# Performance work log

Hardware: AMD Instinct MI355X
Metric: run time of the kernel (lower is better)

The kernel has to match this reference:

```python
import jax, jax.numpy as jnp
import numpy as np

VERY_NEG = -1e30
N_HEADS = 8


def _dag_attention(leaves, ancestors, mask, w1, b1, w2, b2):
    # leaves/ancestors: [C, A, H], mask: [C, A]
    m = mask[..., None]                                   # [C, A, 1]
    x = jnp.concatenate([leaves * m, ancestors * m], -1)  # [C, A, 2H]
    x = jax.nn.relu(x @ w1 + b1)                          # [C, A, H]
    s = x @ w2 + b2 + (1.0 - m) * VERY_NEG                # [C, A, 1]
    a = jax.nn.softmax(s, axis=1)
    return (a * ancestors * m).sum(axis=1)                # [C, H]


def _encoder_layer(x, mask4d, wq, wk, wv, wo, fw1, fb1, fw2, fb2):
    B, S, H = x.shape
    d = H // N_HEADS
    q = (x @ wq).reshape(B, S, N_HEADS, d)
    k = (x @ wk).reshape(B, S, N_HEADS, d)
    v = (x @ wv).reshape(B, S, N_HEADS, d)
    scores = jnp.einsum('bqhd,bkhd->bhqk', q, k) / jnp.sqrt(jnp.float32(d)) + mask4d
    attn = jax.nn.softmax(scores, axis=-1)
    ctx = jnp.einsum('bhqk,bkhd->bqhd', attn, v).reshape(B, S, H)
    x = x + ctx @ wo
    x = x + jax.nn.relu(x @ fw1 + fb1) @ fw2 + fb2
    return x


def _attention_pooling(x, mask3d, pw, pb):
    # x: [B, S, H], mask3d: [B, S, 1] additive mask
    s = x @ pw + pb + mask3d           # [B, S, 1]
    a = jax.nn.softmax(s, axis=1)
    return (a * x).sum(axis=1)          # [B, H]


def setup_inputs() -> dict:
    key = jax.random.key(0)
    ks = jax.random.split(key, 32)
    B, S, H, C, NODES, A = 128, 256, 256, 20000, 25000, 8

    def w(k, shape, scale=0.02):
        return (jax.random.normal(k, shape, jnp.float32) * scale)

    input_ids = jax.random.randint(ks[0], (B, S), 0, C)
    code_mask = (jax.random.uniform(ks[1], (B, S)) < 0.9).astype(jnp.float32)
    code_mask = code_mask.at[:, 0].set(1.0)
    dx_leaves_list = jax.random.randint(ks[2], (C, A), 0, NODES)
    dx_ancestors_list = jax.random.randint(ks[3], (C, A), 0, NODES)
    dx_masks_list = (jax.random.uniform(ks[4], (C, A)) < 0.8).astype(jnp.float32)
    dx_masks_list = dx_masks_list.at[:, 0].set(1.0)

    inp = dict(
        input_ids=input_ids, code_mask=code_mask,
        dx_leaves_list=dx_leaves_list, dx_ancestors_list=dx_ancestors_list,
        dx_masks_list=dx_masks_list,
        embed_init_w=w(ks[5], (NODES + 1, H)).at[NODES].set(0.0),  # padding row
        embed_inputs_w=w(ks[6], (C + 1, H)).at[C].set(0.0),
        attn_w1=w(ks[7], (2 * H, H)), attn_b1=jnp.zeros((H,), jnp.float32),
        attn_w2=w(ks[8], (H, 1)), attn_b2=jnp.zeros((1,), jnp.float32),
        pool_w=w(ks[9], (H, 1)), pool_b=jnp.zeros((1,), jnp.float32),
    )
    names = ['visit', 'dag']
    for i, nm in enumerate(names):
        base = 10 + 6 * i
        inp[nm + '_wq'] = w(ks[base], (H, H))
        inp[nm + '_wk'] = w(ks[base + 1], (H, H))
        inp[nm + '_wv'] = w(ks[base + 2], (H, H))
        inp[nm + '_wo'] = w(ks[base + 3], (H, H))
        inp[nm + '_fw1'] = w(ks[base + 4], (H, 4 * H))
        inp[nm + '_fb1'] = jnp.zeros((4 * H,), jnp.float32)
        inp[nm + '_fw2'] = w(ks[base + 5], (4 * H, H))
        inp[nm + '_fb2'] = jnp.zeros((H,), jnp.float32)
    return inp


def reference(input_ids, code_mask, dx_leaves_list, dx_ancestors_list, dx_masks_list,
              embed_init_w, embed_inputs_w, attn_w1, attn_b1, attn_w2, attn_b2,
              pool_w, pool_b,
              visit_wq, visit_wk, visit_wv, visit_wo, visit_fw1, visit_fb1, visit_fw2, visit_fb2,
              dag_wq, dag_wk, dag_wv, dag_wo, dag_fw1, dag_fb1, dag_fw2, dag_fb2):
    H = embed_init_w.shape[1]
    # Full-vocabulary DAG embedding recomputation (gather -> MLP -> masked softmax -> weighted sum)
    leaves_emb = embed_init_w[dx_leaves_list]          # [C, A, H]
    ancestors_emb = embed_init_w[dx_ancestors_list]    # [C, A, H]
    dag_emb = _dag_attention(leaves_emb, ancestors_emb, dx_masks_list,
                             attn_w1, attn_b1, attn_w2, attn_b2)   # [C, H]
    dict_matrix = jnp.concatenate([jnp.zeros((1, H), jnp.float32), dag_emb], axis=0)

    inputs = embed_inputs_w[input_ids]       # [B, S, H]
    inputs_dag = dict_matrix[input_ids]      # [B, S, H]

    ext_mask = (1.0 - code_mask)[:, None, None, :] * VERY_NEG  # [B,1,1,S]
    visit_outs = _encoder_layer(inputs, ext_mask, visit_wq, visit_wk, visit_wv, visit_wo,
                                visit_fw1, visit_fb1, visit_fw2, visit_fb2)
    dag_hidden = _encoder_layer(inputs_dag, ext_mask, dag_wq, dag_wk, dag_wv, dag_wo,
                                dag_fw1, dag_fb1, dag_fw2, dag_fb2)

    pool_mask = (1.0 - code_mask)[:, :, None] * VERY_NEG       # [B,S,1]
    dag_outs = _attention_pooling(dag_hidden, pool_mask, pool_w, pool_b)
    return (visit_outs, dag_outs)
```

## Files before the change

### kernel.cpp

```cpp
#include <hip/hip_runtime.h>
#include <hip/hip_bf16.h>
#include <math.h>

#define VERY_NEG (-1e30f)

constexpr int Bc = 128, Sc = 256, Hc = 256, Cc = 20000, Ac = 8, NHc = 8, DHc = 32, FFc = 1024;
constexpr int Mc = Bc * Sc;
constexpr int Rc = Cc * Ac;

typedef __attribute__((ext_vector_type(8))) short short8;
typedef __attribute__((ext_vector_type(4))) float floatx4;

static __device__ __forceinline__ unsigned short f2bf(float f) {
  union { float f; unsigned u; } v; v.f = f;
  unsigned r = v.u + 0x7FFF + ((v.u >> 16) & 1);
  return (unsigned short)(r >> 16);
}
static __device__ __forceinline__ unsigned pack2(float lo, float hi) {
  return (unsigned)f2bf(lo) | ((unsigned)f2bf(hi) << 16);
}
static __device__ __forceinline__ float bf2f(unsigned short u) {
  union { unsigned u; float f; } v; v.u = ((unsigned)u) << 16; return v.f;
}

static __device__ __forceinline__ void glds16(const unsigned short* g,
                                              unsigned short* l) {
  __builtin_amdgcn_global_load_lds(
      (const __attribute__((address_space(1))) void*)g,
      (__attribute__((address_space(3))) void*)l, 16, 0, 0);
}

__global__ __launch_bounds__(256) void prep_weights(
    const float* __restrict__ wq, const float* __restrict__ wk,
    const float* __restrict__ wv, const float* __restrict__ wo,
    const float* __restrict__ fw1, const float* __restrict__ fw2,
    unsigned short* __restrict__ qkvT, unsigned short* __restrict__ woT,
    unsigned short* __restrict__ fw1T, unsigned short* __restrict__ fw2T) {
  int gid = blockIdx.x * 256 + threadIdx.x;
  if (gid < 196608) {
    int which = gid >> 16, rem = gid & 65535;
    int n = rem >> 8, k = rem & 255;
    const float* w = which == 0 ? wq : (which == 1 ? wk : wv);
    qkvT[gid] = f2bf(w[k * 256 + n]);
  } else if (gid < 262144) {
    int rem = gid - 196608;
    int n = rem >> 8, k = rem & 255;
    woT[rem] = f2bf(wo[k * 256 + n]);
  } else if (gid < 524288) {
    int rem = gid - 262144;
    int n = rem >> 8, k = rem & 255;
    fw1T[rem] = f2bf(fw1[k * 1024 + n]);
  } else {
    int rem = gid - 524288;
    int n = rem >> 10, k = rem & 1023;
    fw2T[rem] = f2bf(fw2[k * 256 + n]);
  }
}

template <int K, bool BIAS, bool RELU, bool RESID, int OUT>
__global__ __launch_bounds__(256) void gemm_mfma(
    const unsigned short* __restrict__ A, const unsigned short* __restrict__ Bt,
    const float* __restrict__ bias, const float* __restrict__ resid,
    float* __restrict__ Cf, unsigned short* __restrict__ C2, int N) {
  __shared__ unsigned short As[128 * 64];
  __shared__ unsigned short Bs[128 * 64];
  const int tid = threadIdx.x;
  const int rowBase = blockIdx.y * 128;
  const int colBase = blockIdx.x * 128;
  const int wave = tid >> 6, lane = tid & 63;
  const int wm = wave >> 1, wn = wave & 1;
  const int quad = lane >> 4, l15 = lane & 15;
  const int s8 = (((lane & 7) ^ (lane >> 3)) << 3);
  const int rs0 = (wave << 5) + (lane >> 3);
  const int swz = l15 & 7;

  floatx4 acc[4][4];
#pragma unroll
  for (int mt = 0; mt < 4; ++mt)
#pragma unroll
    for (int nt = 0; nt < 4; ++nt) acc[mt][nt] = (floatx4){0.f, 0.f, 0.f, 0.f};

  for (int k0 = 0; k0 < K; k0 += 64) {
#pragma unroll
    for (int i = 0; i < 4; ++i) {
      int r = rs0 + (i << 3);
      int lb = wave * 2048 + i * 512;
      glds16(A + (size_t)(rowBase + r) * K + k0 + s8, &As[lb]);
      glds16(Bt + (size_t)(colBase + r) * K + k0 + s8, &Bs[lb]);
    }
    __syncthreads();
#pragma unroll
    for (int kk = 0; kk < 2; ++kk) {
      short8 af[4], bfr[4];
#pragma unroll
      for (int mt = 0; mt < 4; ++mt)
        af[mt] = *(const short8*)&As[(wm * 64 + mt * 16 + l15) * 64 +
                                     ((((kk << 2) | quad) ^ swz) << 3)];
#pragma unroll
      for (int nt = 0; nt < 4; ++nt)
        bfr[nt] = *(const short8*)&Bs[(wn * 64 + nt * 16 + l15) * 64 +
                                      ((((kk << 2) | quad) ^ swz) << 3)];
#pragma unroll
      for (int mt = 0; mt < 4; ++mt)
#pragma unroll
        for (int nt = 0; nt < 4; ++nt)
          acc[mt][nt] = __builtin_amdgcn_mfma_f32_16x16x32_bf16(
              af[mt], bfr[nt], acc[mt][nt], 0, 0, 0);
    }
    __syncthreads();
  }

#pragma unroll
  for (int mt = 0; mt < 4; ++mt) {
#pragma unroll
    for (int nt = 0; nt < 4; ++nt) {
      int col = colBase + wn * 64 + nt * 16 + l15;
      float bz = BIAS ? bias[col] : 0.f;
#pragma unroll
      for (int i = 0; i < 4; ++i) {
        int row = rowBase + wm * 64 + mt * 16 + quad * 4 + i;
        float v = acc[mt][nt][i];
        if (BIAS) v += bz;
        if (RELU) v = fmaxf(v, 0.f);
        if (RESID) v += resid[(size_t)row * N + col];
        if (OUT == 0) {
          Cf[(size_t)row * N + col] = v;
        } else if (OUT == 1) {
          C2[(size_t)row * N + col] = f2bf(v);
        } else if (OUT == 2) {
          Cf[(size_t)row * N + col] = v;
          C2[(size_t)row * N + col] = f2bf(v);
        } else {
          C2[(size_t)(col >> 8) * 16777216 + (size_t)row * 256 + (col & 255)] =
              f2bf(v);
        }
      }
    }
  }
}

__global__ __launch_bounds__(256) void cvt_emb16(
    const float* __restrict__ emb, unsigned short* __restrict__ e16) {
  int gid = blockIdx.x * 256 + threadIdx.x;
  int base = gid * 8;
  int row = base >> 8;
  uint4 o;
  if (row < 25001) {
    float4 a = *(const float4*)(emb + base);
    float4 b = *(const float4*)(emb + base + 4);
    o.x = pack2(a.x, a.y); o.y = pack2(a.z, a.w);
    o.z = pack2(b.x, b.y); o.w = pack2(b.z, b.w);
  } else {
    o = (uint4){0u, 0u, 0u, 0u};
  }
  *(uint4*)(e16 + base) = o;
}

__global__ __launch_bounds__(256) void prep_w1T_pq(
    const float* __restrict__ w1, unsigned short* __restrict__ Bt) {
  int gid = blockIdx.x * 256 + threadIdx.x;
  int n = gid >> 8, k = gid & 255;
  float v = (n < 256) ? w1[k * 256 + n] : w1[(256 + k) * 256 + (n - 256)];
  Bt[gid] = f2bf(v);
}

__global__ __launch_bounds__(256) void dag_score(
    const int* __restrict__ leaves, const int* __restrict__ anc,
    const unsigned short* __restrict__ PQ, const float* __restrict__ b1,
    const float* __restrict__ w2, float* __restrict__ s) {
  const int tid = threadIdx.x;
  const int l16 = tid & 15;
  const int r = blockIdx.x * 16 + (tid >> 4);

  float b1c[16], w2c[16];
#pragma unroll
  for (int j = 0; j < 4; ++j) {
    *(float4*)&b1c[j * 4] = *(const float4*)(b1 + l16 * 16 + j * 4);
    *(float4*)&w2c[j * 4] = *(const float4*)(w2 + l16 * 16 + j * 4);
  }

  const int nl = leaves[r], na = anc[r];
  const unsigned short* pp = PQ + (size_t)nl * 512 + l16 * 16;
  const unsigned short* qp = PQ + (size_t)na * 512 + 256 + l16 * 16;

  float acc = 0.f;
#pragma unroll
  for (int half = 0; half < 2; ++half) {
    uint4 pv = *(const uint4*)(pp + half * 8);
    uint4 qv = *(const uint4*)(qp + half * 8);
    const unsigned short* pu = (const unsigned short*)&pv;
    const unsigned short* qu = (const unsigned short*)&qv;
#pragma unroll
    for (int j = 0; j < 8; ++j) {
      float h = bf2f(pu[j]) + bf2f(qu[j]) + b1c[half * 8 + j];
      acc += fmaxf(h, 0.f) * w2c[half * 8 + j];
    }
  }
  acc += __shfl_xor(acc, 1, 64);
  acc += __shfl_xor(acc, 2, 64);
  acc += __shfl_xor(acc, 4, 64);
  acc += __shfl_xor(acc, 8, 64);
  if (l16 == 0) s[r] = acc;
}

__global__ __launch_bounds__(256) void dag_finalize(
    const float* __restrict__ s, const float* __restrict__ masks,
    const int* __restrict__ anc, const float* __restrict__ b2,
    const float* __restrict__ emb, float* __restrict__ dict) {
  const int c = blockIdx.x;
  const int t = threadIdx.x;
  __shared__ float sv[8], mv[8];
  __shared__ int nv[8];
  if (t < 8) {
    int idx = c * 8 + t;
    float m = masks[idx];
    sv[t] = s[idx] + b2[0] + (1.f - m) * VERY_NEG;
    mv[t] = m;
    nv[t] = anc[idx];
  }
  __syncthreads();
  float mx = -INFINITY;
#pragma unroll
  for (int a = 0; a < 8; ++a) mx = fmaxf(mx, sv[a]);
  float e[8], sum = 0.f;
#pragma unroll
  for (int a = 0; a < 8; ++a) { e[a] = __expf(sv[a] - mx); sum += e[a]; }
  float inv = 1.f / sum;
  float o = 0.f;
#pragma unroll
  for (int a = 0; a < 8; ++a)
    o += e[a] * inv * mv[a] * emb[(size_t)nv[a] * 256 + t];
  dict[(size_t)(c + 1) * 256 + t] = o;
  if (c == 0) dict[t] = 0.f;
}

__global__ __launch_bounds__(256) void gather_both(
    const int* __restrict__ ids, const float4* __restrict__ table,
    float4* __restrict__ outf, unsigned short* __restrict__ outb) {
  int gid = blockIdx.x * 256 + threadIdx.x;
  int row = gid >> 6;
  int c4 = gid & 63;
  float4 v = table[(size_t)ids[row] * 64 + c4];
  outf[gid] = v;
  uint2 o;
  o.x = pack2(v.x, v.y);
  o.y = pack2(v.z, v.w);
  *(uint2*)(outb + (size_t)gid * 4) = o;
}

__global__ __launch_bounds__(256) void attn_mfma(
    const unsigned short* __restrict__ q, const unsigned short* __restrict__ k,
    const unsigned short* __restrict__ v, const float* __restrict__ cm,
    unsigned short* __restrict__ ctx) {
  __shared__ unsigned short Vt[32][264];
  __shared__ unsigned short Ps[4][64][68];
  __shared__ float madd[256];
  const int b = blockIdx.x >> 3, h = blockIdx.x & 7;
  const int tid = threadIdx.x;
  const int wave = tid >> 6, lane = tid & 63;
  const int quad = lane >> 4, l15 = lane & 15;
  const size_t tokbase = (size_t)b * 256;
  const int hoff = h * 32;

  unsigned short* Vtmp = &Ps[0][0][0];

#pragma unroll
  for (int it = 0; it < 4; ++it) {
    int idx = tid + it * 256;
    int row = idx >> 2, c = idx & 3;
    size_t g = (tokbase + row) * 256 + hoff + c * 8;
    *(uint4*)(Vtmp + row * 40 + c * 8) = *(const uint4*)(v + g);
  }
  madd[tid] = (1.f - cm[b * 256 + tid]) * VERY_NEG;
  __syncthreads();
#pragma unroll
  for (int it = 0; it < 4; ++it) {
    int idx = tid + it * 256;
    int row = idx & 255, c = idx >> 8;
    uint4 w = *(const uint4*)(Vtmp + row * 40 + c * 8);
    const unsigned short* wsp = (const unsigned short*)&w;
#pragma unroll
    for (int j = 0; j < 8; ++j) Vt[c * 8 + j][row] = wsp[j];
  }
  __syncthreads();

  short8 qf[4];
#pragma unroll
  for (int mt = 0; mt < 4; ++mt) {
    size_t qrow = tokbase + wave * 64 + mt * 16 + l15;
    qf[mt] = *(const short8*)(q + qrow * 256 + hoff + quad * 8);
  }
  float madd_r[16];
#pragma unroll
  for (int nt = 0; nt < 16; ++nt) madd_r[nt] = madd[nt * 16 + l15];

  float l_r[4][4];
  floatx4 oa[4][2];
#pragma unroll
  for (int mt = 0; mt < 4; ++mt)
#pragma unroll
    for (int i = 0; i < 4; ++i) l_r[mt][i] = 0.f;
#pragma unroll
  for (int mt = 0; mt < 4; ++mt)
#pragma unroll
    for (int nd = 0; nd < 2; ++nd) oa[mt][nd] = (floatx4){0.f, 0.f, 0.f, 0.f};

  const float scale = 0.17677669529663687f;

  for (int t = 0; t < 4; ++t) {
    short8 kf[4];
#pragma unroll
    for (int nt = 0; nt < 4; ++nt)
      kf[nt] = *(const short8*)(k + (tokbase + t * 64 + nt * 16 + l15) * 256 +
                                hoff + quad * 8);
    floatx4 sa[4][4];
#pragma unroll
    for (int mt = 0; mt < 4; ++mt)
#pragma unroll
      for (int nt = 0; nt < 4; ++nt) sa[mt][nt] = (floatx4){0.f, 0.f, 0.f, 0.f};
#pragma unroll
    for (int mt = 0; mt < 4; ++mt)
#pragma unroll
      for (int nt = 0; nt < 4; ++nt)
        sa[mt][nt] = __builtin_amdgcn_mfma_f32_16x16x32_bf16(
            qf[mt], kf[nt], sa[mt][nt], 0, 0, 0);

#pragma unroll
    for (int mt = 0; mt < 4; ++mt) {
#pragma unroll
      for (int i = 0; i < 4; ++i) {
        float rs = 0.f;
#pragma unroll
        for (int nt = 0; nt < 4; ++nt) {
          float p = __expf(sa[mt][nt][i] * scale + madd_r[t * 4 + nt]);
          sa[mt][nt][i] = p;
          rs += p;
        }
        rs += __shfl_xor(rs, 1, 64);
        rs += __shfl_xor(rs, 2, 64);
        rs += __shfl_xor(rs, 4, 64);
        rs += __shfl_xor(rs, 8, 64);
        l_r[mt][i] += rs;
      }
    }
#pragma unroll
    for (int mt = 0; mt < 4; ++mt)
#pragma unroll
      for (int nt = 0; nt < 4; ++nt)
#pragma unroll
        for (int i = 0; i < 4; ++i)
          Ps[wave][mt * 16 + quad * 4 + i][nt * 16 + l15] =
              f2bf(sa[mt][nt][i]);
    __asm__ __volatile__("s_waitcnt lgkmcnt(0)" ::: "memory");
#pragma unroll
    for (int ks = 0; ks < 2; ++ks) {
      short8 vf[2];
#pragma unroll
      for (int nd = 0; nd < 2; ++nd)
        vf[nd] =
            *(const short8*)&Vt[nd * 16 + l15][t * 64 + ks * 32 + quad * 8];
#pragma unroll
      for (int mt = 0; mt < 4; ++mt) {
        short8 pf = *(const short8*)&Ps[wave][mt * 16 + l15][ks * 32 + quad * 8];
#pragma unroll
        for (int nd = 0; nd < 2; ++nd)
          oa[mt][nd] = __builtin_amdgcn_mfma_f32_16x16x32_bf16(
              pf, vf[nd], oa[mt][nd], 0, 0, 0);
      }
    }
    __asm__ __volatile__("s_waitcnt lgkmcnt(0)" ::: "memory");
  }

  unsigned short* OsW = &Ps[wave][0][0];
#pragma unroll
  for (int mt = 0; mt < 4; ++mt)
#pragma unroll
    for (int nd = 0; nd < 2; ++nd)
#pragma unroll
      for (int i = 0; i < 4; ++i)
        OsW[(mt * 16 + quad * 4 + i) * 40 + nd * 16 + l15] =
            f2bf(oa[mt][nd][i] / l_r[mt][i]);
  __asm__ __volatile__("s_waitcnt lgkmcnt(0)" ::: "memory");
#pragma unroll
  for (int it = 0; it < 4; ++it) {
    int idx = it * 64 + lane;
    int row = idx >> 2, c = idx & 3;
    uint4 w = *(const uint4*)(OsW + row * 40 + c * 8);
    *(uint4*)(ctx + (tokbase + wave * 64 + row) * 256 + hoff + c * 8) = w;
  }
}

__global__ __launch_bounds__(256) void pool_kernel(
    const float* __restrict__ x, const float* __restrict__ code_mask,
    const float* __restrict__ pw, const float* __restrict__ pb,
    float* __restrict__ out) {
  const int b = blockIdx.x;
  const int t = threadIdx.x;
  __shared__ float ss[256];
  __shared__ float red[256];
  __shared__ float als[256];
  const float* xb = x + (size_t)b * 256 * 256;

  float s = pb[0];
  for (int j = 0; j < 256; j += 4) {
    float4 xv = *(const float4*)(xb + (size_t)t * 256 + j);
    float4 wv = *(const float4*)(pw + j);
    s += xv.x * wv.x + xv.y * wv.y + xv.z * wv.z + xv.w * wv.w;
  }
  s += (1.f - code_mask[b * 256 + t]) * VERY_NEG;
  ss[t] = s; red[t] = s;
  __syncthreads();
  for (int off = 128; off > 0; off >>= 1) {
    if (t < off) red[t] = fmaxf(red[t], red[t + off]);
    __syncthreads();
  }
  float m = red[0];
  __syncthreads();
  float e = __expf(ss[t] - m);
  als[t] = e; red[t] = e;
  __syncthreads();
  for (int off = 128; off > 0; off >>= 1) {
    if (t < off) red[t] += red[t + off];
    __syncthreads();
  }
  float inv = 1.f / red[0];
  float o = 0.f;
  for (int si = 0; si < 256; ++si) o += als[si] * xb[(size_t)si * 256 + t];
  out[b * 256 + t] = o * inv;
}

extern "C" void kernel_launch(void* const* d_in, const int* in_sizes, int n_in,
                              void* d_out, int out_size, void* d_ws,
                              size_t ws_size, hipStream_t stream) {
  const int* input_ids = (const int*)d_in[0];
  const float* code_mask = (const float*)d_in[1];
  const int* dx_leaves = (const int*)d_in[2];
  const int* dx_anc = (const int*)d_in[3];
  const float* dx_masks = (const float*)d_in[4];
  const float* embed_init_w = (const float*)d_in[5];
  const float* embed_inputs_w = (const float*)d_in[6];
  const float* attn_w1 = (const float*)d_in[7];
  const float* attn_b1 = (const float*)d_in[8];
  const float* attn_w2 = (const float*)d_in[9];
  const float* attn_b2 = (const float*)d_in[10];
  const float* pool_w = (const float*)d_in[11];
  const float* pool_b = (const float*)d_in[12];

  float* out = (float*)d_out;
  float* ws = (float*)d_ws;

  float* dict = ws;
  float* xbuf = dict + 5120256;
  float* qb   = xbuf + 8388608;
  float* kb   = qb + 8388608;
  float* vb   = kb + 8388608;
  float* ctxb = vb + 8388608;
  float* wend = ctxb + 8388608;

  unsigned short* emb16  = (unsigned short*)xbuf;
  unsigned short* pq16   = (unsigned short*)(xbuf + 3211264);
  unsigned short* w1T_pq = (unsigned short*)kb;
  float* sbuf = vb;

  unsigned short* xb16  = (unsigned short*)ctxb;
  unsigned short* qkv16 = (unsigned short*)qb;
  unsigned short* xq16  = (unsigned short*)qb;
  unsigned short* hid16 = (unsigned short*)kb;
  unsigned short* qkvT = (unsigned short*)wend;
  unsigned short* woT  = qkvT + 196608;
  unsigned short* fw1T = woT + 65536;
  unsigned short* fw2T = fw1T + 262144;

  cvt_emb16<<<3136, 256, 0, stream>>>(embed_init_w, emb16);
  prep_w1T_pq<<<512, 256, 0, stream>>>(attn_w1, w1T_pq);
  gemm_mfma<256, false, false, false, 1><<<dim3(4, 196), 256, 0, stream>>>(
      emb16, w1T_pq, nullptr, nullptr, nullptr, pq16, 512);
  dag_score<<<Rc / 16, 256, 0, stream>>>(dx_leaves, dx_anc, pq16, attn_b1,
                                         attn_w2, sbuf);
  dag_finalize<<<Cc, 256, 0, stream>>>(sbuf, dx_masks, dx_anc, attn_b2,
                                       embed_init_w, dict);

  auto run_encoder = [&](const float* wq, const float* wk, const float* wv,
                         const float* wo, const float* fw1, const float* fb1,
                         const float* fw2, const float* fb2, float* final_out) {
    prep_weights<<<3072, 256, 0, stream>>>(wq, wk, wv, wo, fw1, fw2, qkvT,
                                           woT, fw1T, fw2T);
    gemm_mfma<256, false, false, false, 3><<<dim3(6, 256), 256, 0, stream>>>(
        xb16, qkvT, nullptr, nullptr, nullptr, qkv16, 256);
    attn_mfma<<<Bc * NHc, 256, 0, stream>>>(qkv16, qkv16 + 16777216,
                                            qkv16 + 33554432, code_mask, xb16);
    gemm_mfma<256, false, false, true, 2><<<dim3(2, 256), 256, 0, stream>>>(
        xb16, woT, nullptr, xbuf, xbuf, xq16, 256);
    gemm_mfma<256, true, true, false, 1><<<dim3(8, 256), 256, 0, stream>>>(
        xq16, fw1T, fb1, nullptr, nullptr, hid16, 1024);
    gemm_mfma<1024, true, false, true, 0><<<dim3(2, 256), 256, 0, stream>>>(
        hid16, fw2T, fb2, xbuf, final_out, nullptr, 256);
  };

  gather_both<<<8192, 256, 0, stream>>>(input_ids,
                                        (const float4*)embed_inputs_w,
                                        (float4*)xbuf, xb16);
  run_encoder((const float*)d_in[13], (const float*)d_in[14],
              (const float*)d_in[15], (const float*)d_in[16],
              (const float*)d_in[17], (const float*)d_in[18],
              (const float*)d_in[19], (const float*)d_in[20], out);

  gather_both<<<8192, 256, 0, stream>>>(input_ids, (const float4*)dict,
                                        (float4*)xbuf, xb16);
  run_encoder((const float*)d_in[21], (const float*)d_in[22],
              (const float*)d_in[23], (const float*)d_in[24],
              (const float*)d_in[25], (const float*)d_in[26],
              (const float*)d_in[27], (const float*)d_in[28], xbuf);

  pool_kernel<<<Bc, 256, 0, stream>>>(xbuf, code_mask, pool_w, pool_b,
                                      out + 8388608);
}
```

Measured before the change: 605.2 us.

## Swizzle attention LDS layouts and compute softmax denominators via MFMA

Measured after the change: 582.3 us. 1.04x faster.

```diff
diff --git a/kernel.cpp b/kernel.cpp
--- a/kernel.cpp
+++ b/kernel.cpp
@@ -248,12 +248,19 @@
   *(uint2*)(outb + (size_t)gid * 4) = o;
 }
 
-__global__ __launch_bounds__(256) void attn_mfma(
+static __device__ __forceinline__ int vt_addr(int d, int col) {
+  return d * 272 + ((((col) * 2) ^ (((d >> 3) & 3) << 4)) >> 1);
+}
+static __device__ __forceinline__ int ps_addr(int row, int col) {
+  return row * 40 + ((((col) * 2) ^ (((row >> 2) & 3) << 4)) >> 1);
+}
+
+__global__ __launch_bounds__(256, 4) void attn_mfma(
     const unsigned short* __restrict__ q, const unsigned short* __restrict__ k,
     const unsigned short* __restrict__ v, const float* __restrict__ cm,
     unsigned short* __restrict__ ctx) {
-  __shared__ unsigned short Vt[32][264];
-  __shared__ unsigned short Ps[4][64][68];
+  __shared__ unsigned short Vt[32 * 272];
+  __shared__ unsigned short Ps[4][64 * 40];
   __shared__ float madd[256];
   const int b = blockIdx.x >> 3, h = blockIdx.x & 7;
   const int tid = threadIdx.x;
@@ -262,26 +269,16 @@
   const size_t tokbase = (size_t)b * 256;
   const int hoff = h * 32;
 
-  unsigned short* Vtmp = &Ps[0][0][0];
-
 #pragma unroll
   for (int it = 0; it < 4; ++it) {
     int idx = tid + it * 256;
     int row = idx >> 2, c = idx & 3;
-    size_t g = (tokbase + row) * 256 + hoff + c * 8;
-    *(uint4*)(Vtmp + row * 40 + c * 8) = *(const uint4*)(v + g);
+    uint4 w = *(const uint4*)(v + (tokbase + row) * 256 + hoff + c * 8);
+    const unsigned short* wsp = (const unsigned short*)&w;
+#pragma unroll
+    for (int j = 0; j < 8; ++j) Vt[vt_addr(c * 8 + j, row)] = wsp[j];
   }
   madd[tid] = (1.f - cm[b * 256 + tid]) * VERY_NEG;
-  __syncthreads();
-#pragma unroll
-  for (int it = 0; it < 4; ++it) {
-    int idx = tid + it * 256;
-    int row = idx & 255, c = idx >> 8;
-    uint4 w = *(const uint4*)(Vtmp + row * 40 + c * 8);
-    const unsigned short* wsp = (const unsigned short*)&w;
-#pragma unroll
-    for (int j = 0; j < 8; ++j) Vt[c * 8 + j][row] = wsp[j];
-  }
   __syncthreads();
 
   short8 qf[4];
@@ -294,18 +291,21 @@
 #pragma unroll
   for (int nt = 0; nt < 16; ++nt) madd_r[nt] = madd[nt * 16 + l15];
 
-  float l_r[4][4];
-  floatx4 oa[4][2];
-#pragma unroll
-  for (int mt = 0; mt < 4; ++mt)
-#pragma unroll
-    for (int i = 0; i < 4; ++i) l_r[mt][i] = 0.f;
-#pragma unroll
-  for (int mt = 0; mt < 4; ++mt)
+  short8 vone;
+#pragma unroll
+  for (int j = 0; j < 8; ++j)
+    ((unsigned short*)&vone)[j] = (l15 == 0) ? 0x3F80 : 0;
+
+  floatx4 oa[4][2], oa_l[4];
+#pragma unroll
+  for (int mt = 0; mt < 4; ++mt) {
+    oa_l[mt] = (floatx4){0.f, 0.f, 0.f, 0.f};
 #pragma unroll
     for (int nd = 0; nd < 2; ++nd) oa[mt][nd] = (floatx4){0.f, 0.f, 0.f, 0.f};
+  }
 
   const float scale = 0.17677669529663687f;
+  unsigned short* Pw = &Ps[wave][0];
 
   for (int t = 0; t < 4; ++t) {
     short8 kf[4];
@@ -326,66 +326,59 @@
             qf[mt], kf[nt], sa[mt][nt], 0, 0, 0);
 
 #pragma unroll
-    for (int mt = 0; mt < 4; ++mt) {
-#pragma unroll
-      for (int i = 0; i < 4; ++i) {
-        float rs = 0.f;
-#pragma unroll
-        for (int nt = 0; nt < 4; ++nt) {
-          float p = __expf(sa[mt][nt][i] * scale + madd_r[t * 4 + nt]);
-          sa[mt][nt][i] = p;
-          rs += p;
+    for (int ks = 0; ks < 2; ++ks) {
+#pragma unroll
+      for (int mt = 0; mt < 4; ++mt)
+#pragma unroll
+        for (int n2 = 0; n2 < 2; ++n2) {
+          int nt = ks * 2 + n2;
+#pragma unroll
+          for (int i = 0; i < 4; ++i) {
+            float p = __expf(sa[mt][nt][i] * scale + madd_r[t * 4 + nt]);
+            Pw[ps_addr(mt * 16 + quad * 4 + i, n2 * 16 + l15)] = f2bf(p);
+          }
         }
-        rs += __shfl_xor(rs, 1, 64);
-        rs += __shfl_xor(rs, 2, 64);
-        rs += __shfl_xor(rs, 4, 64);
-        rs += __shfl_xor(rs, 8, 64);
-        l_r[mt][i] += rs;
-      }
-    }
-#pragma unroll
-    for (int mt = 0; mt < 4; ++mt)
-#pragma unroll
-      for (int nt = 0; nt < 4; ++nt)
-#pragma unroll
-        for (int i = 0; i < 4; ++i)
-          Ps[wave][mt * 16 + quad * 4 + i][nt * 16 + l15] =
-              f2bf(sa[mt][nt][i]);
-    __asm__ __volatile__("s_waitcnt lgkmcnt(0)" ::: "memory");
-#pragma unroll
-    for (int ks = 0; ks < 2; ++ks) {
+      __asm__ __volatile__("s_waitcnt lgkmcnt(0)" ::: "memory");
       short8 vf[2];
 #pragma unroll
       for (int nd = 0; nd < 2; ++nd)
-        vf[nd] =
-            *(const short8*)&Vt[nd * 16 + l15][t * 64 + ks * 32 + quad * 8];
+        vf[nd] = *(const short8*)&Vt[vt_addr(nd * 16 + l15,
+                                             t * 64 + ks * 32 + quad * 8)];
 #pragma unroll
       for (int mt = 0; mt < 4; ++mt) {
-        short8 pf = *(const short8*)&Ps[wave][mt * 16 + l15][ks * 32 + quad * 8];
+        short8 pf = *(const short8*)&Pw[ps_addr(mt * 16 + l15, quad * 8)];
 #pragma unroll
         for (int nd = 0; nd < 2; ++nd)
           oa[mt][nd] = __builtin_amdgcn_mfma_f32_16x16x32_bf16(
               pf, vf[nd], oa[mt][nd], 0, 0, 0);
+        oa_l[mt] = __builtin_amdgcn_mfma_f32_16x16x32_bf16(
+            pf, vone, oa_l[mt], 0, 0, 0);
       }
     }
-    __asm__ __volatile__("s_waitcnt lgkmcnt(0)" ::: "memory");
-  }
-
-  unsigned short* OsW = &Ps[wave][0][0];
+  }
+
+  float inv[4][4];
 #pragma unroll
   for (int mt = 0; mt < 4; ++mt)
 #pragma unroll
+    for (int i = 0; i < 4; ++i) {
+      float l = __shfl(oa_l[mt][i], lane & 48, 64);
+      inv[mt][i] = 1.f / l;
+    }
+#pragma unroll
+  for (int mt = 0; mt < 4; ++mt)
+#pragma unroll
     for (int nd = 0; nd < 2; ++nd)
 #pragma unroll
       for (int i = 0; i < 4; ++i)
-        OsW[(mt * 16 + quad * 4 + i) * 40 + nd * 16 + l15] =
-            f2bf(oa[mt][nd][i] / l_r[mt][i]);
+        Pw[ps_addr(mt * 16 + quad * 4 + i, nd * 16 + l15)] =
+            f2bf(oa[mt][nd][i] * inv[mt][i]);
   __asm__ __volatile__("s_waitcnt lgkmcnt(0)" ::: "memory");
 #pragma unroll
   for (int it = 0; it < 4; ++it) {
     int idx = it * 64 + lane;
     int row = idx >> 2, c = idx & 3;
-    uint4 w = *(const uint4*)(OsW + row * 40 + c * 8);
+    uint4 w = *(const uint4*)&Pw[ps_addr(row, c * 8)];
     *(uint4*)(ctx + (tokbase + wave * 64 + row) * 256 + hoff + c * 8) = w;
   }
 }
```
